# Kernel tuning notes

Measured on AMD Instinct MI355X. Metric: run time of the kernel, lower is better.

## Reference

```python
import jax, jax.numpy as jnp
import numpy as np


def kmax_dmp(x, pool_ranges, k_per, K):
    """Vectorized dynamic k-max pooling (order-preserving top-k along time).

    x: [B, T, C] float. pool_ranges: [B] int (per-sample valid prefix length).
    k_per: [B] int (per-sample k, k_per[i] <= pool_ranges[i]). K: static max k.
    Returns [B, K, C]; rows beyond k_per[i] are zero-padded (like pad_sequence).
    """
    B, T, C = x.shape
    neg = jnp.finfo(x.dtype).min
    valid = jnp.arange(T)[None, :] < pool_ranges[:, None]            # [B,T]
    xm = jnp.where(valid[:, :, None], x, neg)
    vals, idx = jax.lax.top_k(jnp.swapaxes(xm, 1, 2), K)             # [B,C,K]
    keep = jnp.arange(K)[None, None, :] < k_per[:, None, None]       # [B,1,K] bcast
    idx = jnp.where(keep, idx, T)                                    # sentinel for dropped slots
    order = jnp.argsort(idx, axis=-1)                                # restore temporal order
    vals = jnp.take_along_axis(vals, order, axis=-1)
    idx = jnp.take_along_axis(idx, order, axis=-1)
    vals = jnp.where(idx < T, vals, jnp.zeros((), x.dtype))          # zero-pad tail
    return jnp.swapaxes(vals, 1, 2)                                  # [B,K,C]


def setup_inputs() -> dict:
    key = jax.random.key(0)
    ks = jax.random.split(key, 8)
    B, T, C = 64, 512, 300
    x = jax.random.normal(ks[0], (B, T, C), jnp.float32)
    lengths = jnp.sort(jax.random.randint(ks[1], (B,), 16, T + 1))[::-1]
    lengths = lengths.at[0].set(T)  # packed sequences are sorted desc; max len == T
    w1 = jax.random.normal(ks[2], (3 * C, 2, 7), jnp.float32) * 0.05        # groups=C//2 -> 2 in-ch/group
    b1 = jax.random.normal(ks[3], (3 * C,), jnp.float32) * 0.05
    w2 = jax.random.normal(ks[4], (14 * C // 4, 2, 6, 5), jnp.float32) * 0.05  # groups=C//4 -> 2 in-ch/group
    b2 = jax.random.normal(ks[5], (14 * C // 4,), jnp.float32) * 0.05
    wfc = jax.random.normal(ks[6], (1, 4 * 14 * C // 4), jnp.float32) * 0.05
    bfc = jax.random.normal(ks[7], (1,), jnp.float32) * 0.05
    return {"x": x, "lengths": lengths, "w1": w1, "b1": b1,
            "w2": w2, "b2": b2, "wfc": wfc, "bfc": bfc}


def reference(x, lengths, w1, b1, w2, b2, wfc, bfc):
    B, T, C = x.shape
    G1, G2 = C // 2, C // 4
    TOP_K, KS1, KS2W = 4, 7, 5
    # zero out padded tail (pad_packed_sequence semantics)
    mask = (jnp.arange(T)[None, :] < lengths[:, None]).astype(x.dtype)
    x = x * mask[:, :, None]
    # grouped conv1d: [B,C,T] -> [B,3C,T+6]
    h = jax.lax.conv_general_dilated(
        jnp.swapaxes(x, 1, 2), w1, (1,), [(KS1 - 1, KS1 - 1)],
        dimension_numbers=("NCH", "OIH", "NCH"), feature_group_count=G1)
    h = h + b1[None, :, None]
    h = jnp.swapaxes(h, 1, 2)                                       # [B,T+6,3C]
    # layer-1 dynamic k-max: k_i = max(top_k, ceil((2-1)/2 * len_i))
    k1 = jnp.maximum(TOP_K, (lengths + 1) // 2)
    K1 = max(TOP_K, (T + 1) // 2)                                   # static (max len == T)
    h = kmax_dmp(h, lengths + (KS1 - 1), k1, K1)                    # [B,K1,3C]
    h = jnp.tanh(jnp.swapaxes(h, 1, 2).reshape(B, G1, 6, K1))       # [B,C//2,6,K1]
    # grouped conv2d: -> [B,14*C//4,1,K1+4]
    h = jax.lax.conv_general_dilated(
        h, w2, (1, 1), [(0, 0), (KS2W - 1, KS2W - 1)],
        dimension_numbers=("NCHW", "OIHW", "NCHW"), feature_group_count=G2)
    h = h + b2[None, :, None, None]
    Wd = K1 + KS2W - 1
    h = h.reshape(B, G2, 14, Wd).transpose(0, 3, 2, 1)              # [B,Wd,14,C//4]
    h = h.reshape(B, Wd, 14 * G2)
    # layer-2 dynamic k-max: k = top_k = 4; valid prefix = k1 + 4
    h = kmax_dmp(h, k1 + (KS2W - 1), jnp.full((B,), TOP_K, lengths.dtype), TOP_K)
    h = jnp.tanh(h).reshape(B, -1)                                  # [B,4*14*C//4]
    out = h @ wfc.T + bfc                                           # [B,1]
    return jnp.concatenate([jnp.zeros_like(out), out], axis=1)      # [B,2]
```

## Files before the change

kernel.cpp:

```cpp
#include <hip/hip_runtime.h>
#include <cstdint>
#include <cstddef>

#define BB   64
#define TT   512
#define CC   300
#define NG1  150
#define OC1  900
#define K1   256
#define RS   264
#define NG2  75

__device__ __forceinline__ unsigned f2key(float f) {
    unsigned u = __float_as_uint(f);
    return (u & 0x80000000u) ? ~u : (u | 0x80000000u);
}
__device__ __forceinline__ float key2f(unsigned k) {
    unsigned u = (k & 0x80000000u) ? (k & 0x7FFFFFFFu) : ~k;
    return __uint_as_float(u);
}
__device__ __forceinline__ float fast_tanh(float x) {
    float e = __expf(2.0f * x);
    return 1.0f - 2.0f * __builtin_amdgcn_rcpf(e + 1.0f);
}
__device__ __forceinline__ int mbcnt64(unsigned long long m) {
    return (int)__builtin_amdgcn_mbcnt_hi((unsigned)(m >> 32),
                 __builtin_amdgcn_mbcnt_lo((unsigned)m, 0u));
}

__global__ void init_out(const float* __restrict__ bfc, float* __restrict__ out) {
    int i = threadIdx.x;
    if (i < 2 * BB) out[i] = (i & 1) ? bfc[0] : 0.0f;
}

template<int S>
__device__ __forceinline__ void conv1_core(
    const float (* __restrict__ xs)[524], int lane, int n, int k,
    const float* wA, const float* wB, float br, float* __restrict__ row)
{
    constexpr int NV = (S == 8) ? 16 : 12;
    const int t0 = S * lane;

    float xa[NV], xb[NV];
    #pragma unroll
    for (int q = 0; q < NV / 4; ++q) {
        *(float4*)&xa[4 * q] = *(const float4*)&xs[0][t0 + 4 * q];
        *(float4*)&xb[4 * q] = *(const float4*)&xs[1][t0 + 4 * q];
    }

    float v[S + 1];
    #pragma unroll
    for (int j = 0; j < S; ++j) {
        float acc = br;
        #pragma unroll
        for (int kk = 0; kk < 7; ++kk)
            acc = fmaf(xa[j + kk], wA[kk], fmaf(xb[j + kk], wB[kk], acc));
        v[j] = (t0 + j < n) ? acc : -INFINITY;
    }
    v[S] = -INFINITY;
    if (S == 8 && n > 512) {
        if (lane < 6 && 512 + lane < n) {
            float acc = br;
            #pragma unroll
            for (int kk = 0; kk < 7; ++kk)
                acc = fmaf(xs[0][512 + lane + kk], wA[kk],
                      fmaf(xs[1][512 + lane + kk], wB[kk], acc));
            v[S] = acc;
        }
    }

    float lmax = -INFINITY, lmin = INFINITY;
    #pragma unroll
    for (int j = 0; j <= S; ++j) {
        lmax = fmaxf(lmax, v[j]);
        lmin = fminf(lmin, (v[j] == -INFINITY) ? INFINITY : v[j]);
    }
    #pragma unroll
    for (int o = 32; o; o >>= 1) {
        lmax = fmaxf(lmax, __shfl_xor(lmax, o));
        lmin = fminf(lmin, __shfl_xor(lmin, o));
    }
    const float vmax = lmax, vmin = lmin;

    float tau; bool found = false;
    int cmax = 0;
    #pragma unroll
    for (int j = 0; j <= S; ++j) cmax += (int)__popcll(__ballot(v[j] == vmax));
    if (cmax >= k) {
        tau = vmax;
    } else {
        float lo = vmin, hi = vmax;
        tau = lo;
        while (true) {
            float mid = 0.5f * (lo + hi);
            if (mid == lo || mid == hi) { tau = lo; break; }
            int c = 0;
            #pragma unroll
            for (int j = 0; j <= S; ++j)
                c += (int)__popcll(__ballot(v[j] >= mid));
            if (c == k) { tau = mid; found = true; break; }
            if (c > k) lo = mid; else hi = mid;
        }
    }

    bool bG[S + 1], bE[S + 1];
    unsigned long long mG[S + 1], mE[S + 1];
    #pragma unroll
    for (int j = 0; j <= S; ++j) {
        bG[j] = found ? (v[j] >= tau) : (v[j] > tau);
        bE[j] = found ? false : (v[j] == tau);
        mG[j] = __ballot(bG[j]);
        mE[j] = __ballot(bE[j]);
    }
    int cg = 0;
    #pragma unroll
    for (int j = 0; j <= S; ++j) cg += (int)__popcll(mG[j]);
    const int budget = k - cg;

    int SGm = 0, SEm = 0, FGm = 0, FEm = 0;
    #pragma unroll
    for (int j = 0; j < S; ++j) {
        SGm += mbcnt64(mG[j]);  FGm += (int)__popcll(mG[j]);
        SEm += mbcnt64(mE[j]);  FEm += (int)__popcll(mE[j]);
    }
    int ownG = 0, ownE = 0;
    #pragma unroll
    for (int j = 0; j < S; ++j) {
        if (bG[j] || bE[j]) {
            int E = SEm + ownE;
            if (bG[j] || E < budget) {
                int pos = SGm + ownG + min(E, budget);
                row[4 + pos] = fast_tanh(v[j]);
            }
        }
        ownG += bG[j] ? 1 : 0;  ownE += bE[j] ? 1 : 0;
    }
    if (S == 8 && (bG[S] || bE[S])) {
        int E = FEm + mbcnt64(mE[S]);
        if (bG[S] || E < budget) {
            int pos = FGm + mbcnt64(mG[S]) + min(E, budget);
            row[4 + pos] = fast_tanh(v[S]);
        }
    }
    if (lane < 4) row[lane] = 0.0f;
    for (int w = k + lane; w < RS - 4; w += 64) row[4 + w] = 0.0f;
}

__global__ __launch_bounds__(384) void conv1_kmax(
    const float* __restrict__ x, const int* __restrict__ lengths,
    const float* __restrict__ w1, const float* __restrict__ b1,
    float* __restrict__ y1)
{
    const int g = blockIdx.x, b = blockIdx.y;
    const int tid = threadIdx.x;
    const int len = lengths[b];
    const int n = len + 6;
    const int k = max(4, (len + 1) >> 1);

    __shared__ __align__(16) float xs[2][524];
    __shared__ float ws[84];
    __shared__ float bs[6];
    if (tid < 84) ws[tid] = w1[g * 84 + tid];
    if (tid < 6)  bs[tid] = b1[g * 6 + tid];
    for (int p = tid; p < 1048; p += 384) {
        int ic = (p >= 524) ? 1 : 0;
        int q = p - ic * 524;
        int t = q - 6;
        xs[ic][q] = (t >= 0 && t < len) ? x[((size_t)b * TT + t) * CC + 2 * g + ic] : 0.0f;
    }
    __syncthreads();

    const int r = tid >> 6, lane = tid & 63;
    float wA[7], wB[7];
    #pragma unroll
    for (int i = 0; i < 7; ++i) { wA[i] = ws[r * 14 + i]; wB[i] = ws[r * 14 + 7 + i]; }
    const float br = bs[r];
    float* row = y1 + ((size_t)b * OC1 + g * 6 + r) * RS;

    if (n <= 256) conv1_core<4>(xs, lane, n, k, wA, wB, br, row);
    else          conv1_core<8>(xs, lane, n, k, wA, wB, br, row);
}

__global__ __launch_bounds__(256) void conv2_kmax_fc(
    const float* __restrict__ y1, const int* __restrict__ lengths,
    const float* __restrict__ w2, const float* __restrict__ b2,
    const float* __restrict__ wfc, float* __restrict__ out)
{
    const int g = blockIdx.x, b = blockIdx.y;
    const int tid = threadIdx.x;
    const int wv = tid >> 6, lane = tid & 63;
    const int len = lengths[b];
    const int k1 = max(4, (len + 1) >> 1);
    const int n2 = k1 + 4;

    const int r2u0 = __builtin_amdgcn_readfirstlane(4 * wv);
    const int nch  = (wv == 3) ? 2 : 4;
    const float* __restrict__ wg = w2 + (size_t)g * 840;
    const float* base = y1 + ((size_t)b * OC1 + g * 12) * RS;

    float bias_s[4];
    #pragma unroll
    for (int it = 0; it < 4; ++it)
        bias_s[it] = (4 * wv + it < 14) ? b2[(size_t)g * 14 + r2u0 + it] : 0.0f;

    float acc[4][4];
    #pragma unroll
    for (int it = 0; it < 4; ++it)
        #pragma unroll
        for (int j = 0; j < 4; ++j) acc[it][j] = bias_s[it];

    for (int c = 0; c < 12; ++c) {
        const float* rp = base + (size_t)c * RS;
        const float4 f0 = *(const float4*)&rp[4 * lane];
        const float4 f1 = *(const float4*)&rp[4 * lane + 4];
        const float e[8] = {f0.x, f0.y, f0.z, f0.w, f1.x, f1.y, f1.z, f1.w};
        #pragma unroll
        for (int it = 0; it < 4; ++it) {
            if (it < nch) {
                const float* wp = wg + (r2u0 + it) * 60 + c * 5;
                #pragma unroll
                for (int kw = 0; kw < 5; ++kw) {
                    const float q = wp[kw];
                    acc[it][0] = fmaf(e[0 + kw], q, acc[it][0]);
                    acc[it][1] = fmaf(e[1 + kw], q, acc[it][1]);
                    acc[it][2] = fmaf(e[2 + kw], q, acc[it][2]);
                    acc[it][3] = fmaf(e[3 + kw], q, acc[it][3]);
                }
            }
        }
    }

    float tval[4];
    #pragma unroll
    for (int it = 0; it < 4; ++it) tval[it] = -INFINITY;
    if (n2 > 256) {
        if (lane < 4 && 256 + lane < n2) {
            const int w = 256 + lane;
            float ta[4];
            #pragma unroll
            for (int it = 0; it < 4; ++it) ta[it] = bias_s[it];
            for (int c = 0; c < 12; ++c) {
                const float* rp = base + (size_t)c * RS;
                #pragma unroll
                for (int kw = 0; kw < 5; ++kw) {
                    const float xv = rp[w + kw];
                    #pragma unroll
                    for (int it = 0; it < 4; ++it)
                        if (it < nch)
                            ta[it] = fmaf(xv, wg[(r2u0 + it) * 60 + c * 5 + kw], ta[it]);
                }
            }
            #pragma unroll
            for (int it = 0; it < 4; ++it) tval[it] = ta[it];
        }
    }

    float fcsum = 0.0f;
    #pragma unroll
    for (int it = 0; it < 4; ++it) {
        if (it < nch) {
            unsigned kk[5];
            #pragma unroll
            for (int j = 0; j < 4; ++j)
                kk[j] = (4 * lane + j < n2) ? f2key(acc[it][j]) : 0u;
            kk[4] = (tval[it] != -INFINITY) ? f2key(tval[it]) : 0u;

            float tv[4]; int ti[4];
            #pragma unroll
            for (int round = 0; round < 4; ++round) {
                unsigned best = max(max(kk[0], kk[1]), max(kk[2], kk[3]));
                best = max(best, kk[4]);
                #pragma unroll
                for (int o = 32; o; o >>= 1)
                    best = max(best, (unsigned)__shfl_xor((int)best, o));
                int jm = 5;
                #pragma unroll
                for (int j = 4; j >= 0; --j) if (kk[j] == best) jm = j;
                unsigned long long m = __ballot(jm < 5);
                int wl;
                if (__popcll(m) == 1) {
                    wl = __ffsll((long long)m) - 1;
                } else {
                    int myt = (jm == 4) ? (256 + lane)
                            : (jm < 4 ? 4 * lane + jm : 0x7FFFFFFF);
                    int tmin = myt;
                    #pragma unroll
                    for (int o = 32; o; o >>= 1) tmin = min(tmin, __shfl_xor(tmin, o));
                    wl = __ffsll((long long)__ballot(myt == tmin)) - 1;
                }
                const int jw = __shfl(jm, wl);
                ti[round] = (jw == 4) ? (256 + wl) : (4 * wl + jw);
                tv[round] = key2f(best);
                #pragma unroll
                for (int j = 0; j < 5; ++j)
                    if (lane == wl && jm == j) kk[j] = 0u;
            }
            #define CSW(a,bq) if (ti[a] > ti[bq]) { int t_=ti[a]; ti[a]=ti[bq]; ti[bq]=t_; float f_=tv[a]; tv[a]=tv[bq]; tv[bq]=f_; }
            CSW(0,1) CSW(2,3) CSW(0,2) CSW(1,3) CSW(1,2)
            #undef CSW

            const float* wfp = wfc + (r2u0 + it) * 75 + g;
            float s = fast_tanh(tv[0]) * wfp[0];
            s = fmaf(fast_tanh(tv[1]), wfp[1050], s);
            s = fmaf(fast_tanh(tv[2]), wfp[2100], s);
            s = fmaf(fast_tanh(tv[3]), wfp[3150], s);
            fcsum += s;
        }
    }
    if (lane == 0) atomicAdd(&out[b * 2 + 1], fcsum);
}

extern "C" void kernel_launch(void* const* d_in, const int* in_sizes, int n_in,
                              void* d_out, int out_size, void* d_ws, size_t ws_size,
                              hipStream_t stream) {
    const float* x       = (const float*)d_in[0];
    const int*   lengths = (const int*)  d_in[1];
    const float* w1      = (const float*)d_in[2];
    const float* b1      = (const float*)d_in[3];
    const float* w2      = (const float*)d_in[4];
    const float* b2      = (const float*)d_in[5];
    const float* wfc     = (const float*)d_in[6];
    const float* bfc     = (const float*)d_in[7];
    float* out = (float*)d_out;
    float* y1  = (float*)d_ws;

    init_out<<<dim3(1), dim3(128), 0, stream>>>(bfc, out);
    conv1_kmax<<<dim3(NG1, BB), dim3(384), 0, stream>>>(x, lengths, w1, b1, y1);
    conv2_kmax_fc<<<dim3(NG2, BB), dim3(256), 0, stream>>>(y1, lengths, w2, b2, wfc, out);
}
```

Before: 335.1 us.

## Fuse conv1+kmax and conv2+kmax+fc into one kernel with LDS intermediate

```diff
diff --git a/kernel.cpp b/kernel.cpp
--- a/kernel.cpp
+++ b/kernel.cpp
@@ -5,8 +5,6 @@
 #define BB   64
 #define TT   512
 #define CC   300
-#define NG1  150
-#define OC1  900
 #define K1   256
 #define RS   264
 #define NG2  75
@@ -143,81 +141,71 @@
         }
     }
     if (lane < 4) row[lane] = 0.0f;
-    for (int w = k + lane; w < RS - 4; w += 64) row[4 + w] = 0.0f;
-}
-
-__global__ __launch_bounds__(384) void conv1_kmax(
+    if (lane < 8) { int idx = 4 + k + lane; if (idx < RS) row[idx] = 0.0f; }
+}
+
+__global__ __launch_bounds__(384) void fused_dcnn(
     const float* __restrict__ x, const int* __restrict__ lengths,
     const float* __restrict__ w1, const float* __restrict__ b1,
-    float* __restrict__ y1)
-{
-    const int g = blockIdx.x, b = blockIdx.y;
-    const int tid = threadIdx.x;
-    const int len = lengths[b];
-    const int n = len + 6;
-    const int k = max(4, (len + 1) >> 1);
-
-    __shared__ __align__(16) float xs[2][524];
-    __shared__ float ws[84];
-    __shared__ float bs[6];
-    if (tid < 84) ws[tid] = w1[g * 84 + tid];
-    if (tid < 6)  bs[tid] = b1[g * 6 + tid];
-    for (int p = tid; p < 1048; p += 384) {
-        int ic = (p >= 524) ? 1 : 0;
-        int q = p - ic * 524;
-        int t = q - 6;
-        xs[ic][q] = (t >= 0 && t < len) ? x[((size_t)b * TT + t) * CC + 2 * g + ic] : 0.0f;
-    }
-    __syncthreads();
-
-    const int r = tid >> 6, lane = tid & 63;
-    float wA[7], wB[7];
-    #pragma unroll
-    for (int i = 0; i < 7; ++i) { wA[i] = ws[r * 14 + i]; wB[i] = ws[r * 14 + 7 + i]; }
-    const float br = bs[r];
-    float* row = y1 + ((size_t)b * OC1 + g * 6 + r) * RS;
-
-    if (n <= 256) conv1_core<4>(xs, lane, n, k, wA, wB, br, row);
-    else          conv1_core<8>(xs, lane, n, k, wA, wB, br, row);
-}
-
-__global__ __launch_bounds__(256) void conv2_kmax_fc(
-    const float* __restrict__ y1, const int* __restrict__ lengths,
     const float* __restrict__ w2, const float* __restrict__ b2,
     const float* __restrict__ wfc, float* __restrict__ out)
 {
-    const int g = blockIdx.x, b = blockIdx.y;
+    const int g   = blockIdx.x;
+    const int b   = blockIdx.y;
     const int tid = threadIdx.x;
-    const int wv = tid >> 6, lane = tid & 63;
+    const int r   = tid >> 6, lane = tid & 63;
     const int len = lengths[b];
-    const int k1 = max(4, (len + 1) >> 1);
-    const int n2 = k1 + 4;
-
-    const int r2u0 = __builtin_amdgcn_readfirstlane(4 * wv);
-    const int nch  = (wv == 3) ? 2 : 4;
+    const int n   = len + 6;
+    const int k   = max(4, (len + 1) >> 1);
+    const int n2  = k + 4;
+
+    __shared__ __align__(16) float xs[4][524];
+    __shared__ __align__(16) float ylds[12][264];
+    __shared__ float partial[6];
+
+    for (int p = tid; p < 4 * 524; p += 384) {
+        int ic = p / 524;
+        int q  = p - ic * 524;
+        int t  = q - 6;
+        xs[ic][q] = (t >= 0 && t < len) ? x[((size_t)b * TT + t) * CC + 4 * g + ic] : 0.0f;
+    }
+    __syncthreads();
+
+    #pragma unroll
+    for (int grp = 0; grp < 2; ++grp) {
+        const float* wp = w1 + ((size_t)(2 * g + grp) * 6 + r) * 14;
+        float wA[7], wB[7];
+        #pragma unroll
+        for (int i = 0; i < 7; ++i) { wA[i] = wp[i]; wB[i] = wp[7 + i]; }
+        const float br = b1[(size_t)(2 * g + grp) * 6 + r];
+        float* row = &ylds[grp * 6 + r][0];
+        if (n <= 256) conv1_core<4>(&xs[2 * grp], lane, n, k, wA, wB, br, row);
+        else          conv1_core<8>(&xs[2 * grp], lane, n, k, wA, wB, br, row);
+    }
+    __syncthreads();
+
+    const int nch = (r < 2) ? 3 : 2;
     const float* __restrict__ wg = w2 + (size_t)g * 840;
-    const float* base = y1 + ((size_t)b * OC1 + g * 12) * RS;
-
-    float bias_s[4];
-    #pragma unroll
-    for (int it = 0; it < 4; ++it)
-        bias_s[it] = (4 * wv + it < 14) ? b2[(size_t)g * 14 + r2u0 + it] : 0.0f;
-
-    float acc[4][4];
-    #pragma unroll
-    for (int it = 0; it < 4; ++it)
+
+    float bias_s[3];
+    #pragma unroll
+    for (int it = 0; it < 3; ++it)
+        bias_s[it] = (it < nch) ? b2[(size_t)g * 14 + (r + 6 * it)] : 0.0f;
+
+    float acc[3][4];
+    #pragma unroll
+    for (int it = 0; it < 3; ++it)
         #pragma unroll
         for (int j = 0; j < 4; ++j) acc[it][j] = bias_s[it];
 
     for (int c = 0; c < 12; ++c) {
-        const float* rp = base + (size_t)c * RS;
-        const float4 f0 = *(const float4*)&rp[4 * lane];
-        const float4 f1 = *(const float4*)&rp[4 * lane + 4];
+        const float4 f0 = *(const float4*)&ylds[c][4 * lane];
+        const float4 f1 = *(const float4*)&ylds[c][4 * lane + 4];
         const float e[8] = {f0.x, f0.y, f0.z, f0.w, f1.x, f1.y, f1.z, f1.w};
         #pragma unroll
-        for (int it = 0; it < 4; ++it) {
+        for (int it = 0; it < 3; ++it) {
             if (it < nch) {
-                const float* wp = wg + (r2u0 + it) * 60 + c * 5;
+                const float* wp = wg + (r + 6 * it) * 60 + c * 5;
                 #pragma unroll
                 for (int kw = 0; kw < 5; ++kw) {
                     const float q = wp[kw];
@@ -230,35 +218,35 @@
         }
     }
 
-    float tval[4];
-    #pragma unroll
-    for (int it = 0; it < 4; ++it) tval[it] = -INFINITY;
+    float tval[3];
+    #pragma unroll
+    for (int it = 0; it < 3; ++it) tval[it] = -INFINITY;
     if (n2 > 256) {
         if (lane < 4 && 256 + lane < n2) {
             const int w = 256 + lane;
-            float ta[4];
-            #pragma unroll
-            for (int it = 0; it < 4; ++it) ta[it] = bias_s[it];
+            float ta[3];
+            #pragma unroll
+            for (int it = 0; it < 3; ++it) ta[it] = bias_s[it];
             for (int c = 0; c < 12; ++c) {
-                const float* rp = base + (size_t)c * RS;
                 #pragma unroll
                 for (int kw = 0; kw < 5; ++kw) {
-                    const float xv = rp[w + kw];
+                    const float xv = ylds[c][w + kw];
                     #pragma unroll
-                    for (int it = 0; it < 4; ++it)
+                    for (int it = 0; it < 3; ++it)
                         if (it < nch)
-                            ta[it] = fmaf(xv, wg[(r2u0 + it) * 60 + c * 5 + kw], ta[it]);
+                            ta[it] = fmaf(xv, wg[(r + 6 * it) * 60 + c * 5 + kw], ta[it]);
                 }
             }
             #pragma unroll
-            for (int it = 0; it < 4; ++it) tval[it] = ta[it];
+            for (int it = 0; it < 3; ++it) tval[it] = ta[it];
         }
     }
 
     float fcsum = 0.0f;
     #pragma unroll
-    for (int it = 0; it < 4; ++it) {
+    for (int it = 0; it < 3; ++it) {
         if (it < nch) {
+            const int r2 = r + 6 * it;
             unsigned kk[5];
             #pragma unroll
             for (int j = 0; j < 4; ++j)
@@ -299,7 +287,7 @@
             CSW(0,1) CSW(2,3) CSW(0,2) CSW(1,3) CSW(1,2)
             #undef CSW
 
-            const float* wfp = wfc + (r2u0 + it) * 75 + g;
+            const float* wfp = wfc + r2 * 75 + g;
             float s = fast_tanh(tv[0]) * wfp[0];
             s = fmaf(fast_tanh(tv[1]), wfp[1050], s);
             s = fmaf(fast_tanh(tv[2]), wfp[2100], s);
@@ -307,7 +295,14 @@
             fcsum += s;
         }
     }
-    if (lane == 0) atomicAdd(&out[b * 2 + 1], fcsum);
+    if (lane == 0) partial[r] = fcsum;
+    __syncthreads();
+    if (tid == 0) {
+        float s = partial[0];
+        #pragma unroll
+        for (int i = 1; i < 6; ++i) s += partial[i];
+        atomicAdd(&out[b * 2 + 1], s);
+    }
 }
 
 extern "C" void kernel_launch(void* const* d_in, const int* in_sizes, int n_in,
@@ -322,9 +317,7 @@
     const float* wfc     = (const float*)d_in[6];
     const float* bfc     = (const float*)d_in[7];
     float* out = (float*)d_out;
-    float* y1  = (float*)d_ws;
 
     init_out<<<dim3(1), dim3(128), 0, stream>>>(bfc, out);
-    conv1_kmax<<<dim3(NG1, BB), dim3(384), 0, stream>>>(x, lengths, w1, b1, y1);
-    conv2_kmax_fc<<<dim3(NG2, BB), dim3(256), 0, stream>>>(y1, lengths, w2, b2, wfc, out);
-}
+    fused_dcnn<<<dim3(NG2, BB), dim3(384), 0, stream>>>(x, lengths, w1, b1, w2, b2, wfc, out);
+}
```

New measurement: 474.5 us. 41.6% more time.
